# Kernel optimization log

Hardware: AMD Instinct MI355X
Metric: run time of the kernel (lower is better)

Reference implementation:

```python
import jax, jax.numpy as jnp
import numpy as np

D_MODEL = 1024
N_HEADS = 16
HEAD_DIM = D_MODEL // N_HEADS
ROPE_THETA = 10000.0


def setup_inputs() -> dict:
    key = jax.random.key(0)
    ks = jax.random.split(key, 5)
    B, S = 4, 2048
    x = jax.random.normal(ks[0], (B, S, D_MODEL), dtype=jnp.float32)
    Wq = jax.random.normal(ks[1], (D_MODEL, D_MODEL), dtype=jnp.float32) * 0.02
    Wk = jax.random.normal(ks[2], (D_MODEL, D_MODEL), dtype=jnp.float32) * 0.02
    Wv = jax.random.normal(ks[3], (D_MODEL, D_MODEL), dtype=jnp.float32) * 0.02
    Wo = jax.random.normal(ks[4], (D_MODEL, D_MODEL), dtype=jnp.float32) * 0.02
    token_positions = jnp.arange(S, dtype=jnp.int32)
    return {"x": x, "token_positions": token_positions, "Wq": Wq, "Wk": Wk, "Wv": Wv, "Wo": Wo}


def apply_rope(t, positions):
    # t: [B, H, S, Dk]; positions: [S]
    half = HEAD_DIM // 2
    inv_freq = 1.0 / (ROPE_THETA ** (jnp.arange(half, dtype=jnp.float32) * 2.0 / HEAD_DIM))
    angles = positions.astype(jnp.float32)[:, None] * inv_freq[None, :]  # [S, half]
    cos = jnp.cos(angles)[None, None]  # [1,1,S,half]
    sin = jnp.sin(angles)[None, None]
    t_even = t[..., 0::2]
    t_odd = t[..., 1::2]
    rot_even = t_even * cos - t_odd * sin
    rot_odd = t_even * sin + t_odd * cos
    out = jnp.stack([rot_even, rot_odd], axis=-1)  # [B,H,S,half,2]
    return out.reshape(t.shape)


def reference(x, token_positions, Wq, Wk, Wv, Wo):
    B, S, _ = x.shape
    H, Dk = N_HEADS, HEAD_DIM
    # QKV projections, split heads -> [B, H, S, Dk]
    q = (x @ Wq).reshape(B, S, H, Dk).transpose(0, 2, 1, 3)
    k = (x @ Wk).reshape(B, S, H, Dk).transpose(0, 2, 1, 3)
    v = (x @ Wv).reshape(B, S, H, Dk).transpose(0, 2, 1, 3)
    q = apply_rope(q, token_positions)
    k = apply_rope(k, token_positions)
    scale = 1.0 / jnp.sqrt(jnp.asarray(Dk, dtype=x.dtype))
    scores = jnp.einsum('bhqd,bhkd->bhqk', q, k) * scale
    causal = jnp.tril(jnp.ones((S, S), dtype=bool))
    scores = jnp.where(causal[None, None], scores, jnp.asarray(-jnp.inf, dtype=scores.dtype))
    attn = jax.nn.softmax(scores, axis=-1)
    ctx = jnp.einsum('bhqk,bhkd->bhqd', attn, v)  # [B,H,S,Dk]
    ctx = ctx.transpose(0, 2, 1, 3).reshape(B, S, H * Dk)
    return ctx @ Wo
```

## Files before the change

### kernel.cpp

```cpp
#include <hip/hip_runtime.h>

typedef unsigned short u16;
typedef unsigned int   u32;
typedef __bf16  bf16x8 __attribute__((ext_vector_type(8)));
typedef float   f32x4  __attribute__((ext_vector_type(4)));
typedef float   f32x16 __attribute__((ext_vector_type(16)));
typedef u16     u16x4  __attribute__((ext_vector_type(4)));
typedef u16     u16x8  __attribute__((ext_vector_type(8)));
typedef u32     u32x4  __attribute__((ext_vector_type(4)));

#define D_MODEL 1024
#define N_HEADS 16
#define HEAD_DIM 64
#define BATCH 4
#define SEQ 2048
#define MROWS (BATCH*SEQ)

__device__ __forceinline__ u16 f2bf(float f){
  unsigned u = __builtin_bit_cast(unsigned, f);
  u += 0x7fffu + ((u >> 16) & 1u);
  return (u16)(u >> 16);
}
__device__ __forceinline__ float bf2f(u16 h){
  unsigned u = ((unsigned)h) << 16;
  return __builtin_bit_cast(float, u);
}
__device__ __forceinline__ u32 cvtpk(float a, float b){
  u32 r; asm("v_cvt_pk_bf16_f32 %0, %1, %2" : "=v"(r) : "v"(a), "v"(b)); return r;
}
__device__ __forceinline__ void gload_lds16(const u16* g, u16* l){
  __builtin_amdgcn_global_load_lds((const __attribute__((address_space(1))) void*)g,
                                   (__attribute__((address_space(3))) void*)l, 16, 0, 0);
}

__global__ void k_cvt_x(const float* __restrict__ x, u16* __restrict__ xb, int n4){
  int i = blockIdx.x * 256 + threadIdx.x;
  if (i >= n4) return;
  float4 v = reinterpret_cast<const float4*>(x)[i];
  u16x4 o;
  o.x = f2bf(v.x); o.y = f2bf(v.y); o.z = f2bf(v.z); o.w = f2bf(v.w);
  *reinterpret_cast<u16x4*>(xb + (size_t)i * 4) = o;
}

__global__ void k_transpose_w(const float* __restrict__ Wq, const float* __restrict__ Wk,
                              const float* __restrict__ Wv, const float* __restrict__ Wo,
                              u16* __restrict__ wt){
  __shared__ float t[32][33];
  int z = blockIdx.z;
  const float* W = (z==0)?Wq:(z==1)?Wk:(z==2)?Wv:Wo;
  u16* O = wt + (size_t)z * (D_MODEL*(size_t)D_MODEL);
  int n0 = blockIdx.x*32, k0 = blockIdx.y*32;
  int tx = threadIdx.x, ty = threadIdx.y;
  #pragma unroll
  for (int i = ty; i < 32; i += 8) t[i][tx] = W[(size_t)(k0+i)*D_MODEL + n0 + tx];
  __syncthreads();
  #pragma unroll
  for (int i = ty; i < 32; i += 8) O[(size_t)(n0+i)*D_MODEL + k0 + tx] = f2bf(t[tx][i]);
}

__global__ void k_rope_tab(const int* __restrict__ pos, float2* __restrict__ tab){
  int i = blockIdx.x * 256 + threadIdx.x;
  int s = i >> 5, f = i & 31;
  float inv = exp2f(-(float)f * (13.287712379549449f / 32.0f));
  float a = (float)pos[s] * inv;
  float sn, cs;
  sincosf(a, &sn, &cs);
  tab[i] = make_float2(cs, sn);
}

template<int MODE>
__global__ __launch_bounds__(256, 4) void k_gemm2(const u16* __restrict__ A, const u16* __restrict__ Bt,
                                                  const float2* __restrict__ tab,
                                                  u16* __restrict__ qout, u16* __restrict__ kout,
                                                  u16* __restrict__ vout, float* __restrict__ fout){
  __shared__ u16 sA0[128*32], sA1[128*32], sB0[128*32], sB1[128*32];
  const int K = 1024;
  int tid = threadIdx.x, lane = tid & 63, w = tid >> 6;
  int lr = lane & 15, lg = lane >> 4;
  int m0 = blockIdx.x * 128, n0 = blockIdx.y * 128;
  int wm = w >> 1, wn = w & 1;
  int srow = lane >> 2, scol = (lane & 3) * 8;
  const u16* ga = A  + (size_t)(m0 + w*16 + srow)*K + scol;
  const u16* gb = Bt + (size_t)(n0 + w*16 + srow)*K + scol;
  f32x4 acc[4][4] = {};

#define STAGE2(t, sa, sb) \
    gload_lds16(ga + (size_t)(t)*32,         sa + (w*16)*32); \
    gload_lds16(ga + (size_t)(t)*32 + 64*K,  sa + (64 + w*16)*32); \
    gload_lds16(gb + (size_t)(t)*32,         sb + (w*16)*32); \
    gload_lds16(gb + (size_t)(t)*32 + 64*K,  sb + (64 + w*16)*32);

#define COMP2(sa, sb) { \
    bf16x8 af[4], bv[4]; \
    _Pragma("unroll") \
    for (int mi = 0; mi < 4; mi++) \
      af[mi] = *(const bf16x8*)&sa[(wm*64 + mi*16 + lr)*32 + lg*8]; \
    _Pragma("unroll") \
    for (int ni = 0; ni < 4; ni++) \
      bv[ni] = *(const bf16x8*)&sb[(wn*64 + ni*16 + lr)*32 + lg*8]; \
    _Pragma("unroll") \
    for (int mi = 0; mi < 4; mi++){ \
      _Pragma("unroll") \
      for (int ni = 0; ni < 4; ni++) \
        acc[mi][ni] = __builtin_amdgcn_mfma_f32_16x16x32_bf16(af[mi], bv[ni], acc[mi][ni], 0, 0, 0); \
    } }

  STAGE2(0, sA0, sB0);
  __syncthreads();
  for (int t2 = 0; t2 < 16; ++t2){
    int t = t2 * 2;
    STAGE2(t+1, sA1, sB1);
    COMP2(sA0, sB0);
    __syncthreads();
    if (t + 2 < 32){ STAGE2(t+2, sA0, sB0); }
    COMP2(sA1, sB1);
    __syncthreads();
  }
#undef STAGE2
#undef COMP2

  #pragma unroll
  for (int mi = 0; mi < 4; mi++){
    int row = m0 + wm*64 + mi*16 + lg*4;
    #pragma unroll
    for (int ni = 0; ni < 4; ni++){
      int col = n0 + wn*64 + ni*16 + lr;
      f32x4 vv = acc[mi][ni];
      if (MODE == 1){
        #pragma unroll
        for (int r = 0; r < 4; r++)
          fout[(size_t)(row + r)*1024 + col] = vv[r];
      } else {
        int cm = col & 1023;
        int hh = cm >> 6, d = cm & 63;
        const int which = n0 >> 10;
        #pragma unroll
        for (int r = 0; r < 4; r++){
          int rr = row + r;
          int bb = rr >> 11, s = rr & (SEQ-1);
          float val = vv[r];
          if (which < 2){
            float partner = __shfl_xor(val, 1);
            float2 cs = tab[s*32 + (d >> 1)];
            float o = (d & 1) ? (partner*cs.y + val*cs.x) : (val*cs.x - partner*cs.y);
            if (which == 0){
              o *= 0.18033688011112042f;
              qout[(size_t)rr*1024 + cm] = f2bf(o);
            } else {
              kout[(((size_t)(bb*N_HEADS + hh))*SEQ + s)*64 + d] = f2bf(o);
            }
          } else {
            vout[(((size_t)(bb*N_HEADS + hh))*(SEQ/16) + (s >> 4))*1024 + d*16 + (s & 15)] = f2bf(val);
          }
        }
      }
    }
  }
}

__global__ __launch_bounds__(64, 3) void k_attn(const u16* __restrict__ q, const u16* __restrict__ k2,
                                                const u16* __restrict__ v2, u16* __restrict__ ctx){
  __shared__ u16 tp[2048];
  const int lane = threadIdx.x;
  const int lq = lane & 31, hl = lane >> 5;
  const int B = blockIdx.x;
  const int bh = B & 63;
  const int qi = 63 - (B >> 6);
  const int b = bh >> 4, h = bh & 15;
  const int q0 = qi * 32;
  const u16* kl = k2 + (size_t)bh*SEQ*64 + (size_t)lq*64 + hl*8;
  const u16* vl = v2 + (size_t)bh*(SEQ/16)*1024 + lq*16 + hl*8;
  const u16* qr_ = q + (size_t)(b*SEQ + q0 + lq)*D_MODEL + h*HEAD_DIM + hl*8;
  bf16x8 qf0 = *(const bf16x8*)&qr_[0];
  bf16x8 qf1 = *(const bf16x8*)&qr_[16];
  bf16x8 qf2 = *(const bf16x8*)&qr_[32];
  bf16x8 qf3 = *(const bf16x8*)&qr_[48];
  f32x16 acc0 = {}, acc1 = {};
  float m = -3.0e38f, l = 0.f;
  bf16x8 kc0 = *(const bf16x8*)&kl[0];
  bf16x8 kc1 = *(const bf16x8*)&kl[16];
  bf16x8 kc2 = *(const bf16x8*)&kl[32];
  bf16x8 kc3 = *(const bf16x8*)&kl[48];

  #pragma unroll 2
  for (int j0 = 0; j0 <= q0; j0 += 32){
    int jn = (j0 + 32 <= q0) ? (j0 + 32) : q0;
    const u16* kn = kl + (size_t)jn*64;
    bf16x8 kn0 = *(const bf16x8*)&kn[0];
    bf16x8 kn1 = *(const bf16x8*)&kn[16];
    bf16x8 kn2 = *(const bf16x8*)&kn[32];
    bf16x8 kn3 = *(const bf16x8*)&kn[48];
    const u16* vr = vl + (size_t)(j0 >> 4)*1024;
    bf16x8 vf00 = *(const bf16x8*)&vr[0];
    bf16x8 vf10 = *(const bf16x8*)&vr[1024];
    bf16x8 vf01 = *(const bf16x8*)&vr[512];
    bf16x8 vf11 = *(const bf16x8*)&vr[1536];

    f32x16 S = {};
    S = __builtin_amdgcn_mfma_f32_32x32x16_bf16(kc0, qf0, S, 0, 0, 0);
    S = __builtin_amdgcn_mfma_f32_32x32x16_bf16(kc1, qf1, S, 0, 0, 0);
    S = __builtin_amdgcn_mfma_f32_32x32x16_bf16(kc2, qf2, S, 0, 0, 0);
    S = __builtin_amdgcn_mfma_f32_32x32x16_bf16(kc3, qf3, S, 0, 0, 0);

    if (j0 == q0){
      #pragma unroll
      for (int r = 0; r < 16; ++r){
        int kk = (r & 3) + 8*(r >> 2) + 4*hl;
        if (kk > lq) S[r] = -3.0e38f;
      }
    }
    float a0 = fmaxf(fmaxf(S[0],S[1]),  fmaxf(S[2],S[3]));
    float a1 = fmaxf(fmaxf(S[4],S[5]),  fmaxf(S[6],S[7]));
    float a2 = fmaxf(fmaxf(S[8],S[9]),  fmaxf(S[10],S[11]));
    float a3 = fmaxf(fmaxf(S[12],S[13]),fmaxf(S[14],S[15]));
    float pm = fmaxf(fmaxf(a0,a1), fmaxf(a2,a3));
    pm = fmaxf(pm, __shfl_xor(pm, 32));
    if (__any(pm > m + 8.f)){
      float mn = fmaxf(m, pm);
      float cr = __builtin_amdgcn_exp2f(m - mn);
      l *= cr;
      #pragma unroll
      for (int r = 0; r < 16; ++r){ acc0[r] *= cr; acc1[r] *= cr; }
      m = mn;
    }
    #pragma unroll
    for (int r = 0; r < 16; ++r) S[r] = __builtin_amdgcn_exp2f(S[r] - m);
    float s0_ = (S[0]+S[1]) + (S[2]+S[3]);
    float s1_ = (S[4]+S[5]) + (S[6]+S[7]);
    float s2_ = (S[8]+S[9]) + (S[10]+S[11]);
    float s3_ = (S[12]+S[13]) + (S[14]+S[15]);
    l += (s0_+s1_) + (s2_+s3_);
    u32 g0a = cvtpk(S[0], S[1]),  g0b = cvtpk(S[2], S[3]);
    u32 g1a = cvtpk(S[4], S[5]),  g1b = cvtpk(S[6], S[7]);
    u32 g2a = cvtpk(S[8], S[9]),  g2b = cvtpk(S[10],S[11]);
    u32 g3a = cvtpk(S[12],S[13]), g3b = cvtpk(S[14],S[15]);
    u32 s0a = hl ? g0a : g1a, s0b = hl ? g0b : g1b;
    u32 e0a = (u32)__shfl_xor((int)s0a, 32), e0b = (u32)__shfl_xor((int)s0b, 32);
    u32 m0a = hl ? g1a : g0a, m0b = hl ? g1b : g0b;
    u32 s1a = hl ? g2a : g3a, s1b = hl ? g2b : g3b;
    u32 e1a = (u32)__shfl_xor((int)s1a, 32), e1b = (u32)__shfl_xor((int)s1b, 32);
    u32 m1a = hl ? g3a : g2a, m1b = hl ? g3b : g2b;
    u32x4 A0 = { hl ? e0a : m0a, hl ? e0b : m0b, hl ? m0a : e0a, hl ? m0b : e0b };
    u32x4 A1 = { hl ? e1a : m1a, hl ? e1b : m1b, hl ? m1a : e1a, hl ? m1b : e1b };
    bf16x8 pa0 = __builtin_bit_cast(bf16x8, A0);
    bf16x8 pa1 = __builtin_bit_cast(bf16x8, A1);
    acc0 = __builtin_amdgcn_mfma_f32_32x32x16_bf16(vf00, pa0, acc0, 0, 0, 0);
    acc0 = __builtin_amdgcn_mfma_f32_32x32x16_bf16(vf10, pa1, acc0, 0, 0, 0);
    acc1 = __builtin_amdgcn_mfma_f32_32x32x16_bf16(vf01, pa0, acc1, 0, 0, 0);
    acc1 = __builtin_amdgcn_mfma_f32_32x32x16_bf16(vf11, pa1, acc1, 0, 0, 0);
    kc0 = kn0; kc1 = kn1; kc2 = kn2; kc3 = kn3;
  }
  l += __shfl_xor(l, 32);
  float inv = __builtin_amdgcn_rcpf(l);
  char* tbc = (char*)tp;
  #pragma unroll
  for (int r = 0; r < 16; ++r){
    int d0 = (r & 3) + 8*(r >> 2) + 4*hl;
    *(u16*)(tbc + lq*128 + ((2*d0)      ^ ((lq & 7) << 4))) = f2bf(acc0[r] * inv);
    *(u16*)(tbc + lq*128 + ((2*(d0+32)) ^ ((lq & 7) << 4))) = f2bf(acc1[r] * inv);
  }
  int qr2 = lane >> 1, chb = (lane & 1) * 4;
  u16* cp = ctx + (size_t)(b*SEQ + q0 + qr2)*D_MODEL + h*HEAD_DIM;
  #pragma unroll
  for (int i = 0; i < 4; ++i){
    int ch = chb + i;
    u16x8 vv = *(const u16x8*)(tbc + qr2*128 + 16*(ch ^ (qr2 & 7)));
    *(u16x8*)&cp[ch*8] = vv;
  }
}

extern "C" void kernel_launch(void* const* d_in, const int* in_sizes, int n_in,
                              void* d_out, int out_size, void* d_ws, size_t ws_size,
                              hipStream_t stream){
  const float* x  = (const float*)d_in[0];
  const int*  pos = (const int*)d_in[1];
  const float* Wq = (const float*)d_in[2];
  const float* Wk = (const float*)d_in[3];
  const float* Wv = (const float*)d_in[4];
  const float* Wo = (const float*)d_in[5];
  float* out = (float*)d_out;
  char* ws = (char*)d_ws;
  u16* xb   = (u16*)(ws);
  u16* wt   = (u16*)(ws + 16777216);
  u16* qb   = (u16*)(ws + 25165824);
  u16* kbh  = (u16*)(ws + 41943040);
  u16* vt2  = (u16*)(ws + 58720256);
  float2* tab = (float2*)(ws + 75497472);
  u16* ctxb = xb;

  k_cvt_x<<<(MROWS*D_MODEL/4)/256, 256, 0, stream>>>(x, xb, MROWS*D_MODEL/4);
  k_transpose_w<<<dim3(32,32,4), dim3(32,8), 0, stream>>>(Wq, Wk, Wv, Wo, wt);
  k_rope_tab<<<(SEQ*32)/256, 256, 0, stream>>>(pos, tab);
  k_gemm2<0><<<dim3(64,24), 256, 0, stream>>>(xb, wt, tab, qb, kbh, vt2, nullptr);
  k_attn<<<dim3(4096), 64, 0, stream>>>(qb, kbh, vt2, ctxb);
  k_gemm2<1><<<dim3(64,8), 256, 0, stream>>>(ctxb, wt + 3145728, nullptr, nullptr, nullptr, nullptr, out);
}
```

Measured before the change: 210.2 us.

## Share double-buffered K/V LDS tiles across four query waves per attention block

The attention kernel moves from one 64-thread wave per 32-query tile to 256-thread blocks, where four waves handle four consecutive query tiles of the same head. K/V tiles are staged into double-buffered shared memory with async global-to-LDS loads and an XOR swizzle, so each tile is fetched once per block instead of once per wave. The aim is to cut redundant global/L2 traffic and hide load latency behind compute. In exchange, every tile step adds a block-wide barrier, and waves with smaller causal ranges sit idle while the block iterates to its largest query tile.

```diff
diff --git a/kernel.cpp b/kernel.cpp
--- a/kernel.cpp
+++ b/kernel.cpp
@@ -158,18 +158,20 @@
   }
 }
 
-__global__ __launch_bounds__(64, 3) void k_attn(const u16* __restrict__ q, const u16* __restrict__ k2,
-                                                const u16* __restrict__ v2, u16* __restrict__ ctx){
-  __shared__ u16 tp[2048];
-  const int lane = threadIdx.x;
+__global__ __launch_bounds__(256, 3) void k_attn(const u16* __restrict__ q, const u16* __restrict__ k2,
+                                                 const u16* __restrict__ v2, u16* __restrict__ ctx){
+  __shared__ u16 kv[2][4096];
+  const int lane = threadIdx.x & 63, w = threadIdx.x >> 6;
   const int lq = lane & 31, hl = lane >> 5;
   const int B = blockIdx.x;
-  const int bh = B & 63;
-  const int qi = 63 - (B >> 6);
+  const int bh = B & 63, g = 15 - (B >> 6);
   const int b = bh >> 4, h = bh & 15;
+  const int qi = 4*g + w;
   const int q0 = qi * 32;
-  const u16* kl = k2 + (size_t)bh*SEQ*64 + (size_t)lq*64 + hl*8;
-  const u16* vl = v2 + (size_t)bh*(SEQ/16)*1024 + lq*16 + hl*8;
+  const int qmax0 = (4*g + 3) * 32;
+  const u16* kglob = k2 + (size_t)bh*SEQ*64;
+  const u16* vglob = v2 + (size_t)bh*(SEQ/16)*1024;
+
   const u16* qr_ = q + (size_t)(b*SEQ + q0 + lq)*D_MODEL + h*HEAD_DIM + hl*8;
   bf16x8 qf0 = *(const bf16x8*)&qr_[0];
   bf16x8 qf1 = *(const bf16x8*)&qr_[16];
@@ -177,82 +179,90 @@
   bf16x8 qf3 = *(const bf16x8*)&qr_[48];
   f32x16 acc0 = {}, acc1 = {};
   float m = -3.0e38f, l = 0.f;
-  bf16x8 kc0 = *(const bf16x8*)&kl[0];
-  bf16x8 kc1 = *(const bf16x8*)&kl[16];
-  bf16x8 kc2 = *(const bf16x8*)&kl[32];
-  bf16x8 kc3 = *(const bf16x8*)&kl[48];
-
-  #pragma unroll 2
-  for (int j0 = 0; j0 <= q0; j0 += 32){
-    int jn = (j0 + 32 <= q0) ? (j0 + 32) : q0;
-    const u16* kn = kl + (size_t)jn*64;
-    bf16x8 kn0 = *(const bf16x8*)&kn[0];
-    bf16x8 kn1 = *(const bf16x8*)&kn[16];
-    bf16x8 kn2 = *(const bf16x8*)&kn[32];
-    bf16x8 kn3 = *(const bf16x8*)&kn[48];
-    const u16* vr = vl + (size_t)(j0 >> 4)*1024;
-    bf16x8 vf00 = *(const bf16x8*)&vr[0];
-    bf16x8 vf10 = *(const bf16x8*)&vr[1024];
-    bf16x8 vf01 = *(const bf16x8*)&vr[512];
-    bf16x8 vf11 = *(const bf16x8*)&vr[1536];
-
-    f32x16 S = {};
-    S = __builtin_amdgcn_mfma_f32_32x32x16_bf16(kc0, qf0, S, 0, 0, 0);
-    S = __builtin_amdgcn_mfma_f32_32x32x16_bf16(kc1, qf1, S, 0, 0, 0);
-    S = __builtin_amdgcn_mfma_f32_32x32x16_bf16(kc2, qf2, S, 0, 0, 0);
-    S = __builtin_amdgcn_mfma_f32_32x32x16_bf16(kc3, qf3, S, 0, 0, 0);
-
-    if (j0 == q0){
+
+  auto STAGE = [&](int bf, int jt){
+    const u16* ks = kglob + (size_t)(jt + (w<<3) + (lane>>3))*64 + (((lane&7)^(lane>>3))<<3);
+    gload_lds16(ks, &kv[bf][w<<9]);
+    const u16* vs = vglob + ((size_t)(jt>>4)<<10) + (w<<9) + (lane<<3);
+    gload_lds16(vs, &kv[bf][2048 + (w<<9)]);
+  };
+
+  STAGE(0, 0);
+  __syncthreads();
+  int p = 0;
+  for (int j0 = 0; j0 <= qmax0; j0 += 32){
+    if (j0 + 32 <= qmax0) STAGE(p^1, j0 + 32);
+    if (j0 <= q0){
+      const char* kb = (const char*)&kv[p][0];
+      bf16x8 kf0 = *(const bf16x8*)(kb + lq*128 + (((0+hl) ^ (lq&7))<<4));
+      bf16x8 kf1 = *(const bf16x8*)(kb + lq*128 + (((2+hl) ^ (lq&7))<<4));
+      bf16x8 kf2 = *(const bf16x8*)(kb + lq*128 + (((4+hl) ^ (lq&7))<<4));
+      bf16x8 kf3 = *(const bf16x8*)(kb + lq*128 + (((6+hl) ^ (lq&7))<<4));
+      const char* vb = kb + 4096;
+      bf16x8 vf00 = *(const bf16x8*)(vb + lq*32 + hl*16);
+      bf16x8 vf01 = *(const bf16x8*)(vb + lq*32 + hl*16 + 1024);
+      bf16x8 vf10 = *(const bf16x8*)(vb + lq*32 + hl*16 + 2048);
+      bf16x8 vf11 = *(const bf16x8*)(vb + lq*32 + hl*16 + 3072);
+
+      f32x16 S = {};
+      S = __builtin_amdgcn_mfma_f32_32x32x16_bf16(kf0, qf0, S, 0, 0, 0);
+      S = __builtin_amdgcn_mfma_f32_32x32x16_bf16(kf1, qf1, S, 0, 0, 0);
+      S = __builtin_amdgcn_mfma_f32_32x32x16_bf16(kf2, qf2, S, 0, 0, 0);
+      S = __builtin_amdgcn_mfma_f32_32x32x16_bf16(kf3, qf3, S, 0, 0, 0);
+
+      if (j0 == q0){
+        #pragma unroll
+        for (int r = 0; r < 16; ++r){
+          int kk = (r & 3) + 8*(r >> 2) + 4*hl;
+          if (kk > lq) S[r] = -3.0e38f;
+        }
+      }
+      float a0 = fmaxf(fmaxf(S[0],S[1]),  fmaxf(S[2],S[3]));
+      float a1 = fmaxf(fmaxf(S[4],S[5]),  fmaxf(S[6],S[7]));
+      float a2 = fmaxf(fmaxf(S[8],S[9]),  fmaxf(S[10],S[11]));
+      float a3 = fmaxf(fmaxf(S[12],S[13]),fmaxf(S[14],S[15]));
+      float pm = fmaxf(fmaxf(a0,a1), fmaxf(a2,a3));
+      pm = fmaxf(pm, __shfl_xor(pm, 32));
+      if (__any(pm > m + 8.f)){
+        float mn = fmaxf(m, pm);
+        float cr = __builtin_amdgcn_exp2f(m - mn);
+        l *= cr;
+        #pragma unroll
+        for (int r = 0; r < 16; ++r){ acc0[r] *= cr; acc1[r] *= cr; }
+        m = mn;
+      }
       #pragma unroll
-      for (int r = 0; r < 16; ++r){
-        int kk = (r & 3) + 8*(r >> 2) + 4*hl;
-        if (kk > lq) S[r] = -3.0e38f;
-      }
+      for (int r = 0; r < 16; ++r) S[r] = __builtin_amdgcn_exp2f(S[r] - m);
+      float s0_ = (S[0]+S[1]) + (S[2]+S[3]);
+      float s1_ = (S[4]+S[5]) + (S[6]+S[7]);
+      float s2_ = (S[8]+S[9]) + (S[10]+S[11]);
+      float s3_ = (S[12]+S[13]) + (S[14]+S[15]);
+      l += (s0_+s1_) + (s2_+s3_);
+      u32 g0a = cvtpk(S[0], S[1]),  g0b = cvtpk(S[2], S[3]);
+      u32 g1a = cvtpk(S[4], S[5]),  g1b = cvtpk(S[6], S[7]);
+      u32 g2a = cvtpk(S[8], S[9]),  g2b = cvtpk(S[10],S[11]);
+      u32 g3a = cvtpk(S[12],S[13]), g3b = cvtpk(S[14],S[15]);
+      u32 s0a = hl ? g0a : g1a, s0b = hl ? g0b : g1b;
+      u32 e0a = (u32)__shfl_xor((int)s0a, 32), e0b = (u32)__shfl_xor((int)s0b, 32);
+      u32 m0a = hl ? g1a : g0a, m0b = hl ? g1b : g0b;
+      u32 s1a = hl ? g2a : g3a, s1b = hl ? g2b : g3b;
+      u32 e1a = (u32)__shfl_xor((int)s1a, 32), e1b = (u32)__shfl_xor((int)s1b, 32);
+      u32 m1a = hl ? g3a : g2a, m1b = hl ? g3b : g2b;
+      u32x4 A0 = { hl ? e0a : m0a, hl ? e0b : m0b, hl ? m0a : e0a, hl ? m0b : e0b };
+      u32x4 A1 = { hl ? e1a : m1a, hl ? e1b : m1b, hl ? m1a : e1a, hl ? m1b : e1b };
+      bf16x8 pa0 = __builtin_bit_cast(bf16x8, A0);
+      bf16x8 pa1 = __builtin_bit_cast(bf16x8, A1);
+      acc0 = __builtin_amdgcn_mfma_f32_32x32x16_bf16(vf00, pa0, acc0, 0, 0, 0);
+      acc0 = __builtin_amdgcn_mfma_f32_32x32x16_bf16(vf10, pa1, acc0, 0, 0, 0);
+      acc1 = __builtin_amdgcn_mfma_f32_32x32x16_bf16(vf01, pa0, acc1, 0, 0, 0);
+      acc1 = __builtin_amdgcn_mfma_f32_32x32x16_bf16(vf11, pa1, acc1, 0, 0, 0);
     }
-    float a0 = fmaxf(fmaxf(S[0],S[1]),  fmaxf(S[2],S[3]));
-    float a1 = fmaxf(fmaxf(S[4],S[5]),  fmaxf(S[6],S[7]));
-    float a2 = fmaxf(fmaxf(S[8],S[9]),  fmaxf(S[10],S[11]));
-    float a3 = fmaxf(fmaxf(S[12],S[13]),fmaxf(S[14],S[15]));
-    float pm = fmaxf(fmaxf(a0,a1), fmaxf(a2,a3));
-    pm = fmaxf(pm, __shfl_xor(pm, 32));
-    if (__any(pm > m + 8.f)){
-      float mn = fmaxf(m, pm);
-      float cr = __builtin_amdgcn_exp2f(m - mn);
-      l *= cr;
-      #pragma unroll
-      for (int r = 0; r < 16; ++r){ acc0[r] *= cr; acc1[r] *= cr; }
-      m = mn;
-    }
-    #pragma unroll
-    for (int r = 0; r < 16; ++r) S[r] = __builtin_amdgcn_exp2f(S[r] - m);
-    float s0_ = (S[0]+S[1]) + (S[2]+S[3]);
-    float s1_ = (S[4]+S[5]) + (S[6]+S[7]);
-    float s2_ = (S[8]+S[9]) + (S[10]+S[11]);
-    float s3_ = (S[12]+S[13]) + (S[14]+S[15]);
-    l += (s0_+s1_) + (s2_+s3_);
-    u32 g0a = cvtpk(S[0], S[1]),  g0b = cvtpk(S[2], S[3]);
-    u32 g1a = cvtpk(S[4], S[5]),  g1b = cvtpk(S[6], S[7]);
-    u32 g2a = cvtpk(S[8], S[9]),  g2b = cvtpk(S[10],S[11]);
-    u32 g3a = cvtpk(S[12],S[13]), g3b = cvtpk(S[14],S[15]);
-    u32 s0a = hl ? g0a : g1a, s0b = hl ? g0b : g1b;
-    u32 e0a = (u32)__shfl_xor((int)s0a, 32), e0b = (u32)__shfl_xor((int)s0b, 32);
-    u32 m0a = hl ? g1a : g0a, m0b = hl ? g1b : g0b;
-    u32 s1a = hl ? g2a : g3a, s1b = hl ? g2b : g3b;
-    u32 e1a = (u32)__shfl_xor((int)s1a, 32), e1b = (u32)__shfl_xor((int)s1b, 32);
-    u32 m1a = hl ? g3a : g2a, m1b = hl ? g3b : g2b;
-    u32x4 A0 = { hl ? e0a : m0a, hl ? e0b : m0b, hl ? m0a : e0a, hl ? m0b : e0b };
-    u32x4 A1 = { hl ? e1a : m1a, hl ? e1b : m1b, hl ? m1a : e1a, hl ? m1b : e1b };
-    bf16x8 pa0 = __builtin_bit_cast(bf16x8, A0);
-    bf16x8 pa1 = __builtin_bit_cast(bf16x8, A1);
-    acc0 = __builtin_amdgcn_mfma_f32_32x32x16_bf16(vf00, pa0, acc0, 0, 0, 0);
-    acc0 = __builtin_amdgcn_mfma_f32_32x32x16_bf16(vf10, pa1, acc0, 0, 0, 0);
-    acc1 = __builtin_amdgcn_mfma_f32_32x32x16_bf16(vf01, pa0, acc1, 0, 0, 0);
-    acc1 = __builtin_amdgcn_mfma_f32_32x32x16_bf16(vf11, pa1, acc1, 0, 0, 0);
-    kc0 = kn0; kc1 = kn1; kc2 = kn2; kc3 = kn3;
+    __syncthreads();
+    p ^= 1;
   }
   l += __shfl_xor(l, 32);
   float inv = __builtin_amdgcn_rcpf(l);
-  char* tbc = (char*)tp;
+  char* tbc = (char*)kv + w*4096;
   #pragma unroll
   for (int r = 0; r < 16; ++r){
     int d0 = (r & 3) + 8*(r >> 2) + 4*hl;
@@ -292,6 +302,6 @@
   k_transpose_w<<<dim3(32,32,4), dim3(32,8), 0, stream>>>(Wq, Wk, Wv, Wo, wt);
   k_rope_tab<<<(SEQ*32)/256, 256, 0, stream>>>(pos, tab);
   k_gemm2<0><<<dim3(64,24), 256, 0, stream>>>(xb, wt, tab, qb, kbh, vt2, nullptr);
-  k_attn<<<dim3(4096), 64, 0, stream>>>(qb, kbh, vt2, ctxb);
+  k_attn<<<dim3(1024), 256, 0, stream>>>(qb, kbh, vt2, ctxb);
   k_gemm2<1><<<dim3(64,8), 256, 0, stream>>>(ctxb, wt + 3145728, nullptr, nullptr, nullptr, nullptr, out);
 }
```

After: 184.1 us. 12.4% less time.
